# Optimization experiments

Measured on AMD Instinct MI355X. Metric: run time of the kernel, lower is better.

## Reference

```python
import jax, jax.numpy as jnp
import numpy as np

N, L, D, ZD, H, C = 128, 256, 256, 128, 8, 32
EPS = 1e-5

def _ln(x, w, b):
    mu = jnp.mean(x, axis=-1, keepdims=True)
    var = jnp.var(x, axis=-1, keepdims=True)
    return (x - mu) * jax.lax.rsqrt(var + EPS) * w + b

def setup_inputs() -> dict:
    key = jax.random.key(0)
    ks = jax.random.split(key, 10)
    s = 0.02
    return {
        "m": jax.random.normal(ks[0], (N, L, D), jnp.float32),
        "z": jax.random.normal(ks[1], (L, L, ZD), jnp.float32),
        "ln1_w": jnp.ones((D,), jnp.float32),
        "ln1_b": jnp.zeros((D,), jnp.float32),
        "wq": jax.random.normal(ks[2], (D, H * C), jnp.float32) * s,
        "wk": jax.random.normal(ks[3], (D, H * C), jnp.float32) * s,
        "wv": jax.random.normal(ks[4], (D, H * C), jnp.float32) * s,
        "lnz_w": jnp.ones((ZD,), jnp.float32),
        "lnz_b": jnp.zeros((ZD,), jnp.float32),
        "wz": jax.random.normal(ks[5], (ZD, H), jnp.float32) * s,
        "wg": jax.random.normal(ks[6], (D, H * C), jnp.float32) * s,
        "bg": jnp.zeros((H * C,), jnp.float32),
        "wo": jax.random.normal(ks[7], (H * C, D), jnp.float32) * s,
        "bo": jnp.zeros((D,), jnp.float32),
    }

def reference(m, z, ln1_w, ln1_b, wq, wk, wv, lnz_w, lnz_b, wz, wg, bg, wo, bo):
    mn = _ln(m, ln1_w, ln1_b)                        # [N,L,D]
    q = (mn @ wq).reshape(N, L, H, C)
    k = (mn @ wk).reshape(N, L, H, C)
    v = (mn @ wv).reshape(N, L, H, C)
    b = _ln(z, lnz_w, lnz_b) @ wz                    # [L,L,H] pair bias
    g = jax.nn.sigmoid(mn @ wg + bg).reshape(N, L, H, C)
    att = jnp.einsum('nqhc,nkhc->nqkh', q, k) * (1.0 / np.sqrt(C)) + b[None]
    att = jax.nn.softmax(att, axis=2)                # over key dim
    o = jnp.einsum('nqkh,nkhc->nqhc', att, v) * g    # gated output
    return o.reshape(N, L, H * C) @ wo + bo          # [N,L,D]
```

## Files before the change

kernel.cpp:

```cpp
#include <hip/hip_runtime.h>
#include <math.h>

typedef unsigned short u16;
typedef unsigned int   u32;
typedef __attribute__((ext_vector_type(8)))  short          bf16x8;
typedef __attribute__((ext_vector_type(4)))  float          f32x4;
typedef __attribute__((ext_vector_type(16))) unsigned short u16x16;

static constexpr int Nn = 128;
static constexpr int Ln = 256;
static constexpr int Dn = 256;
static constexpr int ZDn = 128;
static constexpr int Hn = 8;
static constexpr int Cn = 32;
static constexpr int Mrows = Nn * Ln;
static constexpr float EPS = 1e-5f;
static constexpr int HS = 32768 * 32;

__device__ __forceinline__ float bf_s(u16 u)  { union { u32 i; float f; } x; x.i = ((u32)u) << 16; return x.f; }
__device__ __forceinline__ u32 f2bf(float f) {
  union { float f; u32 i; } x; x.f = f;
  return (x.i + 0x7fffu + ((x.i >> 16) & 1u)) >> 16;
}
__device__ __forceinline__ u32 pk2(float a, float b) { return f2bf(a) | (f2bf(b) << 16); }

__global__ __launch_bounds__(256) void ln_m_kernel(
    const float* __restrict__ x, const float* __restrict__ w,
    const float* __restrict__ b, u16* __restrict__ y)
{
  const int wave = threadIdx.x >> 6;
  const int lane = threadIdx.x & 63;
  const size_t row = (size_t)blockIdx.x * 4 + wave;
  const float4 xv = ((const float4*)(x + row * Dn))[lane];
  float s  = xv.x + xv.y + xv.z + xv.w;
  float s2 = xv.x*xv.x + xv.y*xv.y + xv.z*xv.z + xv.w*xv.w;
  #pragma unroll
  for (int off = 32; off; off >>= 1) {
    s  += __shfl_xor(s, off);
    s2 += __shfl_xor(s2, off);
  }
  const float mu = s * (1.0f / Dn);
  float var = s2 * (1.0f / Dn) - mu * mu;
  var = fmaxf(var, 0.0f);
  const float rstd = rsqrtf(var + EPS);
  const float4 wv = ((const float4*)w)[lane];
  const float4 bv = ((const float4*)b)[lane];
  float4 yv;
  yv.x = (xv.x - mu) * rstd * wv.x + bv.x;
  yv.y = (xv.y - mu) * rstd * wv.y + bv.y;
  yv.z = (xv.z - mu) * rstd * wv.z + bv.z;
  yv.w = (xv.w - mu) * rstd * wv.w + bv.w;
  uint2 p;
  p.x = pk2(yv.x, yv.y);
  p.y = pk2(yv.z, yv.w);
  ((uint2*)(y + row * Dn))[lane] = p;
}

__global__ __launch_bounds__(256) void wcvt_kernel(
    const float* __restrict__ wq, const float* __restrict__ wk,
    const float* __restrict__ wv, const float* __restrict__ wg,
    const float* __restrict__ wo,
    const float* __restrict__ lnz_w, const float* __restrict__ lnz_b,
    const float* __restrict__ wz,
    u16* __restrict__ wcatT, u16* __restrict__ woTh, u16* __restrict__ woTl,
    float* __restrict__ wkhT, float* __restrict__ Sv, float* __restrict__ bsv)
{
  __shared__ float lds[128][8];
  const int bid = blockIdx.x;
  const int t = threadIdx.x;
  if (bid < 1024) {
    const int n = bid & 255, proj = bid >> 8;
    const float* W = proj == 0 ? wq : proj == 1 ? wk : proj == 2 ? wv : wg;
    float v = W[(size_t)t * 256 + n];
    if (proj == 0) v *= 0.17677669529663687f;
    wcatT[(size_t)bid * 256 + t] = (u16)f2bf(v);
  } else if (bid < 1280) {
    const int n = bid - 1024;
    const float x = wo[(size_t)t * 256 + n];
    const u16 h16 = (u16)f2bf(x);
    woTh[(size_t)n * 256 + t] = h16;
    woTl[(size_t)n * 256 + t] = (u16)f2bf(x - bf_s(h16));
  } else {
    if (t < 128) {
      #pragma unroll
      for (int h = 0; h < 8; ++h) {
        const float v = lnz_w[t] * wz[t * 8 + h];
        lds[t][h] = v;
        wkhT[h * 128 + t] = v;
      }
    }
    __syncthreads();
    if (t < 8) {
      float S = 0.0f, bs = 0.0f;
      for (int k = 0; k < 128; ++k) {
        S  += lds[k][t];
        bs += lnz_b[k] * wz[k * 8 + t];
      }
      Sv[t] = S; bsv[t] = bs;
    }
  }
}

__global__ __launch_bounds__(256) void zbias_kernel(
    const float* __restrict__ z, const float* __restrict__ wkhT,
    const float* __restrict__ Sv, const float* __restrict__ bsv,
    float* __restrict__ b2)
{
  __shared__ float zs[64][132];
  __shared__ float wkT_s[8 * 132];
  __shared__ float mu_s[64], rs_s[64];
  const int t = threadIdx.x;
  const int r0 = blockIdx.x * 64;

  #pragma unroll
  for (int u = 0; u < 8; ++u) {
    const int i = u * 256 + t;
    const int row = i >> 5, c4 = i & 31;
    *(float4*)&zs[row][c4 * 4] =
        *(const float4*)(z + (size_t)(r0 + row) * 128 + c4 * 4);
  }
  #pragma unroll
  for (int u = 0; u < 4; ++u) {
    const int i = u * 256 + t;
    wkT_s[(i >> 7) * 132 + (i & 127)] = wkhT[i];
  }
  __syncthreads();

  {
    const int row = t >> 2, q = t & 3;
    float s = 0.0f, s2 = 0.0f;
    #pragma unroll
    for (int u = 0; u < 8; ++u) {
      const float4 v = *(const float4*)&zs[row][(q * 8 + u) * 4];
      s  += v.x + v.y + v.z + v.w;
      s2 += v.x*v.x + v.y*v.y + v.z*v.z + v.w*v.w;
    }
    s += __shfl_xor(s, 1); s2 += __shfl_xor(s2, 1);
    s += __shfl_xor(s, 2); s2 += __shfl_xor(s2, 2);
    if (q == 0) {
      const float mu = s * (1.0f / 128.0f);
      float var = s2 * (1.0f / 128.0f) - mu * mu;
      var = fmaxf(var, 0.0f);
      mu_s[row] = mu;
      rs_s[row] = rsqrtf(var + EPS);
    }
  }
  __syncthreads();

  {
    const int row = t >> 2, hp = t & 3;
    const int h0 = 2 * hp, h1 = 2 * hp + 1;
    float a0 = 0.0f, a1 = 0.0f;
    #pragma unroll
    for (int c4 = 0; c4 < 32; ++c4) {
      const float4 v  = *(const float4*)&zs[row][c4 * 4];
      const float4 w0 = *(const float4*)&wkT_s[h0 * 132 + c4 * 4];
      const float4 w1 = *(const float4*)&wkT_s[h1 * 132 + c4 * 4];
      a0 = fmaf(v.x, w0.x, a0); a0 = fmaf(v.y, w0.y, a0);
      a0 = fmaf(v.z, w0.z, a0); a0 = fmaf(v.w, w0.w, a0);
      a1 = fmaf(v.x, w1.x, a1); a1 = fmaf(v.y, w1.y, a1);
      a1 = fmaf(v.z, w1.z, a1); a1 = fmaf(v.w, w1.w, a1);
    }
    const float mu = mu_s[row], rs = rs_s[row];
    const size_t rg = (size_t)(r0 + row);
    b2[(size_t)h0 * 65536 + rg] = rs * (a0 - mu * Sv[h0]) + bsv[h0];
    b2[(size_t)h1 * 65536 + rg] = rs * (a1 - mu * Sv[h1]) + bsv[h1];
  }
}

__global__ __launch_bounds__(256) void mfma_gemm_qkvg(
    const u16* __restrict__ A, const u16* __restrict__ BT,
    u16* __restrict__ qb, u16* __restrict__ kb,
    u16* __restrict__ vb, u16* __restrict__ gb,
    const float* __restrict__ bg)
{
  __shared__ u16 A_s[128 * 40];
  __shared__ u16 B_s[128 * 40];
  const int t  = threadIdx.x;
  const int w  = t >> 6;
  const int lane = t & 63;
  const int g  = lane >> 4;
  const int li = lane & 15;
  const int m0 = blockIdx.x * 128;
  const int n0 = blockIdx.y * 128;
  const int wr = (w & 1) * 64;
  const int wc = (w >> 1) * 64;
  const int rS = t >> 1, hS = (t & 1) * 16;

  const f32x4 zf = {0.f, 0.f, 0.f, 0.f};
  f32x4 acc[4][4];
  #pragma unroll
  for (int i = 0; i < 4; ++i)
    #pragma unroll
    for (int j = 0; j < 4; ++j) acc[i][j] = zf;

  for (int k0 = 0; k0 < 256; k0 += 32) {
    __syncthreads();
    {
      const uint4* ga = (const uint4*)(A  + (size_t)(m0 + rS) * 256 + k0 + hS);
      const uint4 a0 = ga[0], a1 = ga[1];
      *(uint4*)&A_s[rS * 40 + hS]     = a0;
      *(uint4*)&A_s[rS * 40 + hS + 8] = a1;
      const uint4* gbp = (const uint4*)(BT + (size_t)(n0 + rS) * 256 + k0 + hS);
      const uint4 b0 = gbp[0], b1 = gbp[1];
      *(uint4*)&B_s[rS * 40 + hS]     = b0;
      *(uint4*)&B_s[rS * 40 + hS + 8] = b1;
    }
    __syncthreads();
    bf16x8 af[4], bfr[4];
    #pragma unroll
    for (int i = 0; i < 4; ++i)
      af[i] = *(const bf16x8*)&A_s[(wr + i*16 + li) * 40 + g*8];
    #pragma unroll
    for (int j = 0; j < 4; ++j)
      bfr[j] = *(const bf16x8*)&B_s[(wc + j*16 + li) * 40 + g*8];
    #pragma unroll
    for (int i = 0; i < 4; ++i)
      #pragma unroll
      for (int j = 0; j < 4; ++j)
        acc[i][j] = __builtin_amdgcn_mfma_f32_16x16x32_bf16(af[i], bfr[j], acc[i][j], 0, 0, 0);
  }

  #pragma unroll
  for (int j = 0; j < 4; ++j) {
    const int nglob = n0 + wc + j*16 + li;
    const int proj = nglob >> 8;
    const int h    = (nglob >> 5) & 7;
    const int c    = nglob & 31;
    u16* base = proj == 0 ? qb : proj == 1 ? kb : proj == 2 ? vb : gb;
    const float gbias = (proj == 3) ? bg[h*32 + c] : 0.0f;
    #pragma unroll
    for (int i = 0; i < 4; ++i)
      #pragma unroll
      for (int r = 0; r < 4; ++r) {
        const int m = m0 + wr + i*16 + g*4 + r;
        const float v = acc[i][j][r] + gbias;
        base[(size_t)h * HS + (size_t)m * 32 + c] = (u16)f2bf(v);
      }
  }
}

__global__ __launch_bounds__(256) void attn_mfma_kernel(
    const u16* __restrict__ qb, const u16* __restrict__ kb,
    const u16* __restrict__ vb, const u16* __restrict__ gb,
    const float* __restrict__ b2, u16* __restrict__ obuf)
{
  __shared__ u16 VT_s[32 * 264];
  __shared__ u16 P_s[4 * 32 * 72];

  const int h = blockIdx.x;
  const int n = blockIdx.y;
  const int t = threadIdx.x;
  const int w = t >> 6;
  const int lane = t & 63;
  const int g  = lane >> 4;
  const int li = lane & 15;
  const size_t hb = (size_t)h * HS;
  const size_t rowb = (size_t)n * 256;

  {
    const u16* vg = vb + hb + (rowb + t) * 32;
    const u16x16 v0 = *(const u16x16*)vg;
    const u16x16 v1 = *(const u16x16*)(vg + 16);
    #pragma unroll
    for (int c = 0; c < 16; ++c) {
      VT_s[c * 264 + t]        = v0[c];
      VT_s[(c + 16) * 264 + t] = v1[c];
    }
  }

  bf16x8 qfrag[4];
  #pragma unroll
  for (int qt = 0; qt < 4; ++qt)
    qfrag[qt] = *(const bf16x8*)(qb + hb + (rowb + w*64 + qt*16 + li) * 32 + g*8);

  __syncthreads();

  const f32x4 zf = {0.f, 0.f, 0.f, 0.f};
  f32x4 oacc[4][2];
  #pragma unroll
  for (int qt = 0; qt < 4; ++qt) { oacc[qt][0] = zf; oacc[qt][1] = zf; }
  float lpart[4][4] = {};
  const int woff = w * 32 * 72;

  for (int k0 = 0; k0 < 256; k0 += 64) {
    #pragma unroll
    for (int qh = 0; qh < 2; ++qh) {
      #pragma unroll
      for (int kt = 0; kt < 4; ++kt) {
        const int krow = k0 + kt*16 + li;
        const bf16x8 kfrag = *(const bf16x8*)(kb + hb + (rowb + krow) * 32 + g*8);
        #pragma unroll
        for (int qq = 0; qq < 2; ++qq) {
          const int qt = qh*2 + qq;
          f32x4 s = __builtin_amdgcn_mfma_f32_16x16x32_bf16(qfrag[qt], kfrag, zf, 0, 0, 0);
          const int qlo = w*64 + qt*16 + g*4;
          const float* bp = b2 + ((size_t)h << 16) + (size_t)qlo * 256 + (k0 + kt*16 + li);
          #pragma unroll
          for (int r = 0; r < 4; ++r) {
            float sv = s[r] + bp[(size_t)r * 256];
            sv = fminf(fmaxf(sv, -30.0f), 30.0f);
            const float p = __expf(sv);
            lpart[qt][r] += p;
            P_s[woff + (qq*16 + g*4 + r) * 72 + kt*16 + li] = (u16)f2bf(p);
          }
        }
      }
      __syncthreads();
      #pragma unroll
      for (int ks = 0; ks < 2; ++ks) {
        bf16x8 afr0 = *(const bf16x8*)&P_s[woff + (li)      * 72 + ks*32 + g*8];
        bf16x8 afr1 = *(const bf16x8*)&P_s[woff + (16 + li) * 72 + ks*32 + g*8];
        #pragma unroll
        for (int ct = 0; ct < 2; ++ct) {
          const bf16x8 vfr = *(const bf16x8*)&VT_s[(ct*16 + li) * 264 + k0 + ks*32 + g*8];
          oacc[qh*2+0][ct] = __builtin_amdgcn_mfma_f32_16x16x32_bf16(afr0, vfr, oacc[qh*2+0][ct], 0, 0, 0);
          oacc[qh*2+1][ct] = __builtin_amdgcn_mfma_f32_16x16x32_bf16(afr1, vfr, oacc[qh*2+1][ct], 0, 0, 0);
        }
      }
      __syncthreads();
    }
  }

  #pragma unroll
  for (int qt = 0; qt < 4; ++qt)
    #pragma unroll
    for (int r = 0; r < 4; ++r) {
      float l = lpart[qt][r];
      l += __shfl_xor(l, 1);
      l += __shfl_xor(l, 2);
      l += __shfl_xor(l, 4);
      l += __shfl_xor(l, 8);
      lpart[qt][r] = 1.0f / l;
    }

  #pragma unroll
  for (int qt = 0; qt < 4; ++qt)
    #pragma unroll
    for (int ct = 0; ct < 2; ++ct)
      #pragma unroll
      for (int r = 0; r < 4; ++r) {
        const int q = w*64 + qt*16 + g*4 + r;
        const int c = ct*16 + li;
        const float gpre = bf_s(gb[hb + (rowb + q) * 32 + c]);
        const float gate = 1.0f / (1.0f + __expf(-gpre));
        obuf[(rowb + q) * 256 + h*32 + c] =
            (u16)f2bf(oacc[qt][ct][r] * lpart[qt][r] * gate);
      }
}

__global__ __launch_bounds__(256) void out_proj_kernel(
    const u16* __restrict__ Abuf, const u16* __restrict__ woT,
    const float* __restrict__ bo, float* __restrict__ out)
{
  __shared__ u16 A_s[64 * 264];
  __shared__ u16 B_s[256 * 40];
  const int t  = threadIdx.x;
  const int w  = t >> 6;
  const int lane = t & 63;
  const int g  = lane >> 4;
  const int li = lane & 15;
  const int m0 = blockIdx.x * 64;
  const int wr = (w & 1) * 32;
  const int wc = (w >> 1) * 128;

  #pragma unroll
  for (int j = 0; j < 8; ++j) {
    const int u = j * 256 + t;
    const int row = u >> 5, c8 = u & 31;
    *(uint4*)&A_s[row * 264 + c8 * 8] =
        *(const uint4*)(Abuf + (size_t)(m0 + row) * 256 + c8 * 8);
  }

  const f32x4 zf = {0.f, 0.f, 0.f, 0.f};
  f32x4 acc[2][8];
  #pragma unroll
  for (int i = 0; i < 2; ++i)
    #pragma unroll
    for (int j = 0; j < 8; ++j) acc[i][j] = zf;

  for (int k0 = 0; k0 < 256; k0 += 32) {
    __syncthreads();
    {
      const u16* sh = woT + (size_t)t * 256 + k0;
      #pragma unroll
      for (int u = 0; u < 4; ++u)
        *(uint4*)&B_s[t * 40 + u*8] = *(const uint4*)(sh + u*8);
    }
    __syncthreads();
    bf16x8 af[2];
    #pragma unroll
    for (int i = 0; i < 2; ++i)
      af[i] = *(const bf16x8*)&A_s[(wr + i*16 + li) * 264 + k0 + g*8];
    #pragma unroll
    for (int j = 0; j < 8; ++j) {
      const bf16x8 bfr = *(const bf16x8*)&B_s[(wc + j*16 + li) * 40 + g*8];
      #pragma unroll
      for (int i = 0; i < 2; ++i)
        acc[i][j] = __builtin_amdgcn_mfma_f32_16x16x32_bf16(af[i], bfr, acc[i][j], 0, 0, 0);
    }
  }

  #pragma unroll
  for (int j = 0; j < 8; ++j) {
    const int col = wc + j*16 + li;
    const float bias = bo[col];
    #pragma unroll
    for (int i = 0; i < 2; ++i)
      #pragma unroll
      for (int r = 0; r < 4; ++r) {
        const int m = m0 + wr + i*16 + g*4 + r;
        out[(size_t)m * 256 + col] = acc[i][j][r] + bias;
      }
  }
}

extern "C" void kernel_launch(void* const* d_in, const int* in_sizes, int n_in,
                              void* d_out, int out_size, void* d_ws, size_t ws_size,
                              hipStream_t stream)
{
  const float* m     = (const float*)d_in[0];
  const float* z     = (const float*)d_in[1];
  const float* ln1_w = (const float*)d_in[2];
  const float* ln1_b = (const float*)d_in[3];
  const float* wq    = (const float*)d_in[4];
  const float* wk    = (const float*)d_in[5];
  const float* wv    = (const float*)d_in[6];
  const float* lnz_w = (const float*)d_in[7];
  const float* lnz_b = (const float*)d_in[8];
  const float* wz    = (const float*)d_in[9];
  const float* wg    = (const float*)d_in[10];
  const float* bg    = (const float*)d_in[11];
  const float* wo    = (const float*)d_in[12];
  const float* bo    = (const float*)d_in[13];
  float* out = (float*)d_out;

  char* ws = (char*)d_ws;
  const size_t MB = 1024 * 1024;
  u16*   mn    = (u16*)(ws);
  u16*   qb    = (u16*)(ws + 16*MB);
  u16*   kb    = (u16*)(ws + 32*MB);
  u16*   vb    = (u16*)(ws + 48*MB);
  u16*   gb    = (u16*)(ws + 64*MB);
  float* b2    = (float*)(ws + 80*MB);
  u16*   wcatT = (u16*)(ws + 82*MB);
  u16*   woTh  = (u16*)(ws + 82*MB + 512*1024);
  u16*   woTl  = (u16*)(ws + 82*MB + 640*1024);
  float* wkhT  = (float*)(ws + 82*MB + 768*1024);
  float* Sv    = (float*)(ws + 82*MB + 772*1024);
  float* bsv   = (float*)(ws + 82*MB + 773*1024);
  u16*   obuf  = mn;

  wcvt_kernel<<<1281, 256, 0, stream>>>(wq, wk, wv, wg, wo, lnz_w, lnz_b, wz,
                                        wcatT, woTh, woTl, wkhT, Sv, bsv);
  ln_m_kernel<<<Mrows/4, 256, 0, stream>>>(m, ln1_w, ln1_b, mn);
  zbias_kernel<<<(Ln*Ln)/64, 256, 0, stream>>>(z, wkhT, Sv, bsv, b2);

  mfma_gemm_qkvg<<<dim3(Mrows/128, 1024/128), 256, 0, stream>>>(
      mn, wcatT, qb, kb, vb, gb, bg);

  attn_mfma_kernel<<<dim3(Hn, Nn), 256, 0, stream>>>(qb, kb, vb, gb, b2, obuf);

  out_proj_kernel<<<Mrows/64, 256, 0, stream>>>(obuf, woTh, bo, out);
}
```

Baseline: 138.9 us.

## Fold log2e into weights, use exp2 without clamp, and load GEMM tiles directly to LDS

The change folds log2(e) into the Q scaling, the pair-bias rstd and the bias sum, so the attention softmax can call the hardware exp2 directly and drop the clamp and the exp scaling. Separately, the QKVG GEMM stages its A and B tiles with global_load_lds direct-to-LDS transfers instead of register round-trips, and drops the row padding from 40 to 32. Removing the padding may add LDS bank conflicts on the fragment reads. Removing the clamp relies on the scores never overflowing, since there is no max subtraction.

```diff
diff --git a/kernel.cpp b/kernel.cpp
--- a/kernel.cpp
+++ b/kernel.cpp
@@ -15,6 +15,7 @@
 static constexpr int Cn = 32;
 static constexpr int Mrows = Nn * Ln;
 static constexpr float EPS = 1e-5f;
+static constexpr float LOG2E = 1.4426950408889634f;
 static constexpr int HS = 32768 * 32;
 
 __device__ __forceinline__ float bf_s(u16 u)  { union { u32 i; float f; } x; x.i = ((u32)u) << 16; return x.f; }
@@ -72,7 +73,7 @@
     const int n = bid & 255, proj = bid >> 8;
     const float* W = proj == 0 ? wq : proj == 1 ? wk : proj == 2 ? wv : wg;
     float v = W[(size_t)t * 256 + n];
-    if (proj == 0) v *= 0.17677669529663687f;
+    if (proj == 0) v *= 0.17677669529663687f * LOG2E;
     wcatT[(size_t)bid * 256 + t] = (u16)f2bf(v);
   } else if (bid < 1280) {
     const int n = bid - 1024;
@@ -96,7 +97,7 @@
         S  += lds[k][t];
         bs += lnz_b[k] * wz[k * 8 + t];
       }
-      Sv[t] = S; bsv[t] = bs;
+      Sv[t] = S; bsv[t] = LOG2E * bs;
     }
   }
 }
@@ -161,7 +162,8 @@
       a1 = fmaf(v.x, w1.x, a1); a1 = fmaf(v.y, w1.y, a1);
       a1 = fmaf(v.z, w1.z, a1); a1 = fmaf(v.w, w1.w, a1);
     }
-    const float mu = mu_s[row], rs = rs_s[row];
+    const float mu = mu_s[row];
+    const float rs = rs_s[row] * LOG2E;
     const size_t rg = (size_t)(r0 + row);
     b2[(size_t)h0 * 65536 + rg] = rs * (a0 - mu * Sv[h0]) + bsv[h0];
     b2[(size_t)h1 * 65536 + rg] = rs * (a1 - mu * Sv[h1]) + bsv[h1];
@@ -174,8 +176,8 @@
     u16* __restrict__ vb, u16* __restrict__ gb,
     const float* __restrict__ bg)
 {
-  __shared__ u16 A_s[128 * 40];
-  __shared__ u16 B_s[128 * 40];
+  __shared__ u16 A_s[128 * 32];
+  __shared__ u16 B_s[128 * 32];
   const int t  = threadIdx.x;
   const int w  = t >> 6;
   const int lane = t & 63;
@@ -185,7 +187,6 @@
   const int n0 = blockIdx.y * 128;
   const int wr = (w & 1) * 64;
   const int wc = (w >> 1) * 64;
-  const int rS = t >> 1, hS = (t & 1) * 16;
 
   const f32x4 zf = {0.f, 0.f, 0.f, 0.f};
   f32x4 acc[4][4];
@@ -196,24 +197,30 @@
 
   for (int k0 = 0; k0 < 256; k0 += 32) {
     __syncthreads();
-    {
-      const uint4* ga = (const uint4*)(A  + (size_t)(m0 + rS) * 256 + k0 + hS);
-      const uint4 a0 = ga[0], a1 = ga[1];
-      *(uint4*)&A_s[rS * 40 + hS]     = a0;
-      *(uint4*)&A_s[rS * 40 + hS + 8] = a1;
-      const uint4* gbp = (const uint4*)(BT + (size_t)(n0 + rS) * 256 + k0 + hS);
-      const uint4 b0 = gbp[0], b1 = gbp[1];
-      *(uint4*)&B_s[rS * 40 + hS]     = b0;
-      *(uint4*)&B_s[rS * 40 + hS + 8] = b1;
+    #pragma unroll
+    for (int i = 0; i < 2; ++i) {
+      const int cb  = (i*4 + w) * 1024 + lane * 16;
+      const int row = cb >> 6;
+      const int ku  = (cb & 63) >> 1;
+      __builtin_amdgcn_global_load_lds(
+          (const __attribute__((address_space(1))) void*)
+              (A + (size_t)(m0 + row) * 256 + k0 + ku),
+          (__attribute__((address_space(3))) void*)(A_s + (i*4 + w) * 512),
+          16, 0, 0);
+      __builtin_amdgcn_global_load_lds(
+          (const __attribute__((address_space(1))) void*)
+              (BT + (size_t)(n0 + row) * 256 + k0 + ku),
+          (__attribute__((address_space(3))) void*)(B_s + (i*4 + w) * 512),
+          16, 0, 0);
     }
     __syncthreads();
     bf16x8 af[4], bfr[4];
     #pragma unroll
     for (int i = 0; i < 4; ++i)
-      af[i] = *(const bf16x8*)&A_s[(wr + i*16 + li) * 40 + g*8];
+      af[i] = *(const bf16x8*)&A_s[(wr + i*16 + li) * 32 + g*8];
     #pragma unroll
     for (int j = 0; j < 4; ++j)
-      bfr[j] = *(const bf16x8*)&B_s[(wc + j*16 + li) * 40 + g*8];
+      bfr[j] = *(const bf16x8*)&B_s[(wc + j*16 + li) * 32 + g*8];
     #pragma unroll
     for (int i = 0; i < 4; ++i)
       #pragma unroll
@@ -298,9 +305,7 @@
           const float* bp = b2 + ((size_t)h << 16) + (size_t)qlo * 256 + (k0 + kt*16 + li);
           #pragma unroll
           for (int r = 0; r < 4; ++r) {
-            float sv = s[r] + bp[(size_t)r * 256];
-            sv = fminf(fmaxf(sv, -30.0f), 30.0f);
-            const float p = __expf(sv);
+            const float p = __builtin_amdgcn_exp2f(s[r] + bp[(size_t)r * 256]);
             lpart[qt][r] += p;
             P_s[woff + (qq*16 + g*4 + r) * 72 + kt*16 + li] = (u16)f2bf(p);
           }
```

Measured after the change: 135.4 us. 1.03x faster.
